# Kernel optimization log

Hardware: AMD Instinct MI355X
Metric: run time of the kernel (lower is better)

Reference implementation:

```python
import jax, jax.numpy as jnp
import numpy as np

B, IN_CH, OUT_CH = 4, 64, 128
N_HIGH, N_LOW = 163842, 40962
GROUPS, EPS, SLOPE = 4, 1e-5, 0.2


def setup_inputs() -> dict:
    key = jax.random.key(0)
    ks = jax.random.split(key, 6)
    x = jax.random.normal(ks[0], (B, IN_CH, N_HIGH), jnp.float32)
    pool_neigh = jax.random.randint(ks[1], (N_LOW * 7,), 0, N_HIGH, dtype=jnp.int32)
    conv_neigh = jax.random.randint(ks[2], (N_LOW * 7,), 0, N_LOW, dtype=jnp.int32)
    W1 = jax.random.normal(ks[3], (OUT_CH, 7 * IN_CH), jnp.float32) / np.float32(np.sqrt(7 * IN_CH))
    b1 = jnp.zeros((OUT_CH,), jnp.float32)
    W2 = jax.random.normal(ks[4], (OUT_CH, 7 * OUT_CH), jnp.float32) / np.float32(np.sqrt(7 * OUT_CH))
    b2 = jnp.zeros((OUT_CH,), jnp.float32)
    return dict(x=x, pool_neigh=pool_neigh, conv_neigh=conv_neigh,
                W1=W1, b1=b1, gn1_w=jnp.ones((OUT_CH,), jnp.float32), gn1_b=jnp.zeros((OUT_CH,), jnp.float32),
                W2=W2, b2=b2, gn2_w=jnp.ones((OUT_CH,), jnp.float32), gn2_b=jnp.zeros((OUT_CH,), jnp.float32))


def _mean_pool(x, pool_neigh):
    # x: (B, C, N_high); pool_neigh: (N_low*7,) -> (B, C, N_low)
    g = x[:, :, pool_neigh].reshape(x.shape[0], x.shape[1], -1, 7)
    return g.mean(axis=-1)


def _onering_conv(x, neigh, W, b):
    # x: (B, C, N); neigh: (N*7,); W: (O, 7*C). Torch Linear over gathered
    # (N*7, C).view(N, 7*C): neighbor-major, channel-minor concatenation.
    Bb, C, N = x.shape
    feat = x[:, :, neigh].reshape(Bb, C, N, 7)            # (B, C, N, 7)
    feat = jnp.transpose(feat, (0, 2, 3, 1)).reshape(Bb, N, 7 * C)  # (B, N, 7C)
    out = jnp.einsum('bnf,of->bno', feat, W) + b          # (B, N, O)
    return jnp.transpose(out, (0, 2, 1))                  # (B, O, N)


def _group_norm(x, w, b):
    # x: (B, C, N), normalize per (group, sample) over (C//G, N)
    Bb, C, N = x.shape
    xg = x.reshape(Bb, GROUPS, C // GROUPS, N)
    mu = xg.mean(axis=(2, 3), keepdims=True)
    var = ((xg - mu) ** 2).mean(axis=(2, 3), keepdims=True)
    xn = ((xg - mu) * jax.lax.rsqrt(var + EPS)).reshape(Bb, C, N)
    return xn * w[None, :, None] + b[None, :, None]


def _leaky_relu(x):
    return jnp.where(x >= 0, x, SLOPE * x)


def reference(x, pool_neigh, conv_neigh, W1, b1, gn1_w, gn1_b, W2, b2, gn2_w, gn2_b):
    h = _mean_pool(x, pool_neigh)
    h = _leaky_relu(_group_norm(_onering_conv(h, conv_neigh, W1, b1), gn1_w, gn1_b))
    h = _leaky_relu(_group_norm(_onering_conv(h, conv_neigh, W2, b2), gn2_w, gn2_b))
    return h
```

## Files before the change

### kernel.cpp

```cpp
#include <hip/hip_runtime.h>

#define B_SZ 4
#define IN_CH 64
#define OUT_CH 128
#define NHI 163842
#define NLO 40962
#define EPS_GN 1e-5f
#define SLOPE 0.2f

typedef __attribute__((ext_vector_type(8))) short short8;
typedef __attribute__((ext_vector_type(16))) float f32x16;

__device__ inline ushort f2bf(float f) {
    union { float f; unsigned u; } v; v.f = f;
    unsigned r = v.u + 0x7FFF + ((v.u >> 16) & 1);
    return (ushort)(r >> 16);
}
__device__ inline float bf2f(ushort h) {
    union { unsigned u; float f; } v; v.u = ((unsigned)h) << 16;
    return v.f;
}

__global__ void k_transpose_x(const float* __restrict__ x, ushort* __restrict__ xT) {
    __shared__ float t[64][65];
    const int b   = blockIdx.y;
    const int n0  = blockIdx.x * 64;
    const int tid = threadIdx.x;
    const int nq  = tid & 15;
    const int c0  = tid >> 4;
    const bool full = (n0 + 64) <= NHI;
    if (full) {
#pragma unroll
        for (int r = 0; r < 4; ++r) {
            int c = c0 + r * 16;
            float4 v = *(const float4*)&x[((long)b * IN_CH + c) * NHI + n0 + nq * 4];
            t[c][nq * 4 + 0] = v.x; t[c][nq * 4 + 1] = v.y;
            t[c][nq * 4 + 2] = v.z; t[c][nq * 4 + 3] = v.w;
        }
    } else {
        for (int r = 0; r < 4; ++r) {
            int c = c0 + r * 16;
            for (int e = 0; e < 4; ++e) {
                int n = n0 + nq * 4 + e;
                t[c][nq * 4 + e] = (n < NHI) ? x[((long)b * IN_CH + c) * NHI + n] : 0.f;
            }
        }
    }
    __syncthreads();
    const int n  = tid >> 2;
    const int cc = (tid & 3) * 16;
    if (n0 + n < NHI) {
        short8 o0, o1;
#pragma unroll
        for (int e = 0; e < 8; ++e) {
            o0[e] = (short)f2bf(t[cc + e][n]);
            o1[e] = (short)f2bf(t[cc + 8 + e][n]);
        }
        ushort* p = &xT[((long)b * NHI + n0 + n) * 64 + cc];
        *(short8*)p = o0;
        *(short8*)(p + 8) = o1;
    }
}

__global__ void k_prep_w(const float* __restrict__ W, ushort* __restrict__ Wb, int K) {
    int i = blockIdx.x * 256 + threadIdx.x;
    if (i >= K * 128) return;
    int k = i / 128, o = i % 128;
    int step = k >> 6, kk = k & 63, kg = kk >> 3, e = kk & 7;
    Wb[(((long)(step * 8 + kg) * 128 + o) * 8) + e] = f2bf(W[(long)o * K + k]);
}

__global__ void k_pool(const ushort* __restrict__ xT, const int* __restrict__ pn,
                       ushort* __restrict__ h1) {
    long t = (long)blockIdx.x * 256 + threadIdx.x;
    const long total = (long)B_SZ * NLO * 8;
    if (t >= total) return;
    int  cq = (int)(t & 7);
    long bn = t >> 3;
    int  n  = (int)(bn % NLO);
    int  b  = (int)(bn / NLO);
    float acc[8] = {};
#pragma unroll
    for (int j = 0; j < 7; ++j) {
        int idx = pn[n * 7 + j];
        short8 v = *(const short8*)&xT[((long)b * NHI + idx) * 64 + cq * 8];
#pragma unroll
        for (int e = 0; e < 8; ++e) acc[e] += bf2f((ushort)v[e]);
    }
    short8 o;
#pragma unroll
    for (int e = 0; e < 8; ++e) o[e] = (short)f2bf(acc[e] * (1.f / 7.f));
    *(short8*)&h1[bn * 64 + cq * 8] = o;
}

template <int CIN>
__global__ __launch_bounds__(256)
void k_conv_mfma(const ushort* __restrict__ src, const int* __restrict__ nbr,
                 const ushort* __restrict__ Wb, const float* __restrict__ bias,
                 ushort* __restrict__ out, float* __restrict__ part) {
    constexpr int K = 7 * CIN;
    constexpr int NSTEP = K / 64;
    __shared__ ushort Asm[8 * 64 * 8];
    __shared__ ushort Bsm[8 * 128 * 8];
    __shared__ float  red[4][4];

    const int b    = blockIdx.y;
    const int n0   = blockIdx.x * 64;
    const int tid  = threadIdx.x;
    const int lane = tid & 63;
    const int wave = tid >> 6;
    const int wr   = wave >> 1, wc = wave & 1;

    const int s_nn = tid >> 2;
    const int s_kq = tid & 3;
    int nrow = n0 + s_nn; if (nrow >= NLO) nrow = NLO - 1;
    const int* nbr_row = &nbr[nrow * 7];

    f32x16 acc0 = {}; f32x16 acc1 = {};
    const long srcb = (long)b * NLO * CIN;

    const int arow  = wr * 32 + (lane & 31);
    const int bcol0 = wc * 64 + (lane & 31);
    const int khalf = lane >> 5;

    for (int step = 0; step < NSTEP; ++step) {
        int j, cbase;
        if (CIN == 64) { j = step; cbase = 0; }
        else           { j = step >> 1; cbase = (step & 1) * 64; }
        int row = nbr_row[j];
        const ushort* sp = &src[srcb + (long)row * CIN + cbase + s_kq * 8];
        short8 a0 = *(const short8*)sp;
        short8 a1 = *(const short8*)(sp + 32);
        const ushort* wp = &Wb[(long)step * 8192 + tid * 32];
        short8 w0 = *(const short8*)(wp);
        short8 w1 = *(const short8*)(wp + 8);
        short8 w2 = *(const short8*)(wp + 16);
        short8 w3 = *(const short8*)(wp + 24);
        __syncthreads();
        *(short8*)&Asm[(s_kq * 64 + s_nn) * 8]       = a0;
        *(short8*)&Asm[((s_kq + 4) * 64 + s_nn) * 8] = a1;
        *(short8*)&Bsm[tid * 32]      = w0;
        *(short8*)&Bsm[tid * 32 + 8]  = w1;
        *(short8*)&Bsm[tid * 32 + 16] = w2;
        *(short8*)&Bsm[tid * 32 + 24] = w3;
        __syncthreads();
#pragma unroll
        for (int kh = 0; kh < 4; ++kh) {
            int kg = 2 * kh + khalf;
            short8 af  = *(const short8*)&Asm[(kg * 64 + arow) * 8];
            short8 bf0 = *(const short8*)&Bsm[(kg * 128 + bcol0) * 8];
            short8 bf1 = *(const short8*)&Bsm[(kg * 128 + bcol0 + 32) * 8];
            acc0 = __builtin_amdgcn_mfma_f32_32x32x16_bf16(af, bf0, acc0, 0, 0, 0);
            acc1 = __builtin_amdgcn_mfma_f32_32x32x16_bf16(af, bf1, acc1, 0, 0, 0);
        }
    }

    const float bias0 = bias[wc * 64 + (lane & 31)];
    const float bias1 = bias[wc * 64 + 32 + (lane & 31)];
    float s0 = 0.f, q0 = 0.f, s1 = 0.f, q1 = 0.f;
#pragma unroll
    for (int r = 0; r < 16; ++r) {
        int rrow = (r & 3) + 8 * (r >> 2) + 4 * khalf + wr * 32;
        int n = n0 + rrow;
        float v0 = acc0[r] + bias0;
        float v1 = acc1[r] + bias1;
        if (n < NLO) {
            long o = ((long)b * NLO + n) * 128 + wc * 64 + (lane & 31);
            out[o]      = f2bf(v0);
            out[o + 32] = f2bf(v1);
            s0 += v0; q0 += v0 * v0;
            s1 += v1; q1 += v1 * v1;
        }
    }
#pragma unroll
    for (int off = 32; off > 0; off >>= 1) {
        s0 += __shfl_down(s0, off); q0 += __shfl_down(q0, off);
        s1 += __shfl_down(s1, off); q1 += __shfl_down(q1, off);
    }
    if (lane == 0) { red[wave][0] = s0; red[wave][1] = q0; red[wave][2] = s1; red[wave][3] = q1; }
    __syncthreads();
    if (tid < 8) {
        int g = tid >> 1, isq = tid & 1;
        int wcg = g >> 1, ct = g & 1;
        float v = red[0 * 2 + wcg][ct * 2 + isq] + red[1 * 2 + wcg][ct * 2 + isq];
        part[(((long)b * gridDim.x + blockIdx.x) * 4 + g) * 2 + isq] = v;
    }
}

__global__ void k_finalize(const float* __restrict__ part, int nblk,
                           const float* __restrict__ w, const float* __restrict__ bb,
                           float* __restrict__ scale, float* __restrict__ shift) {
    const int b = blockIdx.x >> 2, g = blockIdx.x & 3;
    const int tid = threadIdx.x;
    float s = 0.f, ss = 0.f;
    for (int k = tid; k < nblk; k += 256) {
        s  += part[(((long)b * nblk + k) * 4 + g) * 2 + 0];
        ss += part[(((long)b * nblk + k) * 4 + g) * 2 + 1];
    }
#pragma unroll
    for (int off = 32; off > 0; off >>= 1) {
        s += __shfl_down(s, off); ss += __shfl_down(ss, off);
    }
    __shared__ float red[8];
    __shared__ float fin[2];
    const int wave = tid >> 6, lane = tid & 63;
    if (lane == 0) { red[wave * 2] = s; red[wave * 2 + 1] = ss; }
    __syncthreads();
    if (tid == 0) {
        float as = red[0] + red[2] + red[4] + red[6];
        float aq = red[1] + red[3] + red[5] + red[7];
        const float cnt = 32.f * NLO;
        float mu  = as / cnt;
        float var = aq / cnt - mu * mu;
        fin[0] = mu; fin[1] = rsqrtf(var + EPS_GN);
    }
    __syncthreads();
    if (tid < 32) {
        int c = g * 32 + tid;
        float sc = fin[1] * w[c];
        scale[b * 128 + c] = sc;
        shift[b * 128 + c] = bb[c] - fin[0] * sc;
    }
}

__global__ void k_gnapply(const ushort* __restrict__ y, const float* __restrict__ sc,
                          const float* __restrict__ sh, ushort* __restrict__ yp) {
    long t = (long)blockIdx.x * 256 + threadIdx.x;
    const long total = (long)B_SZ * NLO * 16;
    if (t >= total) return;
    int  c8 = (int)(t & 15);
    long bn = t >> 4;
    int  b  = (int)(bn / NLO);
    short8 v = *(const short8*)&y[bn * 128 + c8 * 8];
    short8 o;
#pragma unroll
    for (int e = 0; e < 8; ++e) {
        int c = c8 * 8 + e;
        float f = bf2f((ushort)v[e]) * sc[b * 128 + c] + sh[b * 128 + c];
        f = (f >= 0.f) ? f : SLOPE * f;
        o[e] = (short)f2bf(f);
    }
    *(short8*)&yp[bn * 128 + c8 * 8] = o;
}

__global__ void k_output(const ushort* __restrict__ y2, const float* __restrict__ scale,
                         const float* __restrict__ shift, float* __restrict__ out) {
    __shared__ float t[32][129];
    const int b   = blockIdx.y;
    const int n0  = blockIdx.x * 32;
    const int tid = threadIdx.x;
    const float* scb = &scale[b * 128];
    const float* shb = &shift[b * 128];
    const int c8 = (tid & 15) * 8;
#pragma unroll
    for (int r = 0; r < 2; ++r) {
        int nn = (tid >> 4) + r * 16;
        int n  = n0 + nn;
        if (n < NLO) {
            short8 v = *(const short8*)&y2[((long)b * NLO + n) * 128 + c8];
#pragma unroll
            for (int e = 0; e < 8; ++e) {
                int c = c8 + e;
                float f = bf2f((ushort)v[e]) * scb[c] + shb[c];
                t[nn][c] = (f >= 0.f) ? f : SLOPE * f;
            }
        } else {
#pragma unroll
            for (int e = 0; e < 8; ++e) t[nn][c8 + e] = 0.f;
        }
    }
    __syncthreads();
    const int n4 = (tid & 7) * 4;
    const bool full = (n0 + 32) <= NLO;
#pragma unroll
    for (int r = 0; r < 4; ++r) {
        int c = (tid >> 3) + r * 32;
        long o = ((long)b * 128 + c) * NLO + n0 + n4;
        if (full) {
            float2 v0 = make_float2(t[n4][c], t[n4 + 1][c]);
            float2 v1 = make_float2(t[n4 + 2][c], t[n4 + 3][c]);
            *(float2*)&out[o]     = v0;
            *(float2*)&out[o + 2] = v1;
        } else {
            for (int e = 0; e < 4; ++e)
                if (n0 + n4 + e < NLO) out[o + e] = t[n4 + e][c];
        }
    }
}

extern "C" void kernel_launch(void* const* d_in, const int* in_sizes, int n_in,
                              void* d_out, int out_size, void* d_ws, size_t ws_size,
                              hipStream_t stream) {
    const float* x   = (const float*)d_in[0];
    const int*   pn  = (const int*)d_in[1];
    const int*   cn  = (const int*)d_in[2];
    const float* W1  = (const float*)d_in[3];
    const float* b1  = (const float*)d_in[4];
    const float* g1w = (const float*)d_in[5];
    const float* g1b = (const float*)d_in[6];
    const float* W2  = (const float*)d_in[7];
    const float* b2  = (const float*)d_in[8];
    const float* g2w = (const float*)d_in[9];
    const float* g2b = (const float*)d_in[10];
    float* out = (float*)d_out;
    char*  base = (char*)d_ws;

    ushort* xT  = (ushort*)(base + 0);
    ushort* y1  = (ushort*)(base + 0);
    ushort* y1p = (ushort*)(base + 44000000);
    ushort* h1  = (ushort*)(base + 88000000);
    ushort* y2  = (ushort*)(base + 110000000);
    ushort* wb1 = (ushort*)(base + 152000000);
    ushort* wb2 = (ushort*)(base + 152200000);
    float*  p1  = (float*)(base + 152500000);
    float*  p2  = (float*)(base + 152600000);
    float*  sc1 = (float*)(base + 152700000);
    float*  sh1 = sc1 + 512;
    float*  sc2 = (float*)(base + 152710000);
    float*  sh2 = sc2 + 512;

    const int NBLK = (NLO + 63) / 64;

    k_transpose_x<<<dim3((NHI + 63) / 64, B_SZ), 256, 0, stream>>>(x, xT);
    k_prep_w<<<(448 * 128 + 255) / 256, 256, 0, stream>>>(W1, wb1, 448);
    k_prep_w<<<(896 * 128 + 255) / 256, 256, 0, stream>>>(W2, wb2, 896);
    k_pool<<<(int)(((long)B_SZ * NLO * 8 + 255) / 256), 256, 0, stream>>>(xT, pn, h1);
    k_conv_mfma<64><<<dim3(NBLK, B_SZ), 256, 0, stream>>>(h1, cn, wb1, b1, y1, p1);
    k_finalize<<<16, 256, 0, stream>>>(p1, NBLK, g1w, g1b, sc1, sh1);
    k_gnapply<<<(int)(((long)B_SZ * NLO * 16 + 255) / 256), 256, 0, stream>>>(y1, sc1, sh1, y1p);
    k_conv_mfma<128><<<dim3(NBLK, B_SZ), 256, 0, stream>>>(y1p, cn, wb2, b2, y2, p2);
    k_finalize<<<16, 256, 0, stream>>>(p2, NBLK, g2w, g2b, sc2, sh2);
    k_output<<<dim3((NLO + 31) / 32, B_SZ), 256, 0, stream>>>(y2, sc2, sh2, out);
}
```

Before: 267.5 us.

## Double-buffer conv MFMA tiles with register prefetch and widen to 128-row blocks

The one-ring conv kernel now handles 128 output rows per block with 512 threads instead of 64 rows with 256. Shared memory for the A and B tiles is double-buffered. Global loads for the next K step are issued into registers right after the barrier, so they overlap the current step's MFMAs, and each step needs one barrier instead of two. Each block loads its weight chunk once for twice as many rows, halving weight reloads, though the larger LDS footprint and thread count may reduce how many blocks fit on a CU. Leaky ReLU is also rewritten as fmaxf(f, slope*f) in the GroupNorm apply and output kernels.

```diff
diff --git a/kernel.cpp b/kernel.cpp
--- a/kernel.cpp
+++ b/kernel.cpp
@@ -94,18 +94,18 @@
 }
 
 template <int CIN>
-__global__ __launch_bounds__(256)
+__global__ __launch_bounds__(512, 4)
 void k_conv_mfma(const ushort* __restrict__ src, const int* __restrict__ nbr,
                  const ushort* __restrict__ Wb, const float* __restrict__ bias,
                  ushort* __restrict__ out, float* __restrict__ part) {
     constexpr int K = 7 * CIN;
     constexpr int NSTEP = K / 64;
-    __shared__ ushort Asm[8 * 64 * 8];
-    __shared__ ushort Bsm[8 * 128 * 8];
-    __shared__ float  red[4][4];
+    __shared__ ushort Asm[2][8 * 128 * 8];
+    __shared__ ushort Bsm[2][8 * 128 * 8];
+    __shared__ float  red[8][4];
 
     const int b    = blockIdx.y;
-    const int n0   = blockIdx.x * 64;
+    const int n0   = blockIdx.x * 128;
     const int tid  = threadIdx.x;
     const int lane = tid & 63;
     const int wave = tid >> 6;
@@ -116,40 +116,48 @@
     int nrow = n0 + s_nn; if (nrow >= NLO) nrow = NLO - 1;
     const int* nbr_row = &nbr[nrow * 7];
 
-    f32x16 acc0 = {}; f32x16 acc1 = {};
+    f32x16 acc0 = {}, acc1 = {};
     const long srcb = (long)b * NLO * CIN;
 
     const int arow  = wr * 32 + (lane & 31);
     const int bcol0 = wc * 64 + (lane & 31);
     const int khalf = lane >> 5;
 
+    short8 a0, a1, w0, w1;
+    {
+        int j = 0, cbase = 0;
+        const ushort* sp = &src[srcb + (long)nbr_row[j] * CIN + cbase + s_kq * 8];
+        a0 = *(const short8*)sp;
+        a1 = *(const short8*)(sp + 32);
+        const ushort* wp = &Wb[tid * 16];
+        w0 = *(const short8*)wp;
+        w1 = *(const short8*)(wp + 8);
+    }
+
     for (int step = 0; step < NSTEP; ++step) {
-        int j, cbase;
-        if (CIN == 64) { j = step; cbase = 0; }
-        else           { j = step >> 1; cbase = (step & 1) * 64; }
-        int row = nbr_row[j];
-        const ushort* sp = &src[srcb + (long)row * CIN + cbase + s_kq * 8];
-        short8 a0 = *(const short8*)sp;
-        short8 a1 = *(const short8*)(sp + 32);
-        const ushort* wp = &Wb[(long)step * 8192 + tid * 32];
-        short8 w0 = *(const short8*)(wp);
-        short8 w1 = *(const short8*)(wp + 8);
-        short8 w2 = *(const short8*)(wp + 16);
-        short8 w3 = *(const short8*)(wp + 24);
+        const int cur = step & 1;
+        *(short8*)&Asm[cur][(s_kq * 128 + s_nn) * 8]       = a0;
+        *(short8*)&Asm[cur][((s_kq + 4) * 128 + s_nn) * 8] = a1;
+        *(short8*)&Bsm[cur][tid * 16]     = w0;
+        *(short8*)&Bsm[cur][tid * 16 + 8] = w1;
         __syncthreads();
-        *(short8*)&Asm[(s_kq * 64 + s_nn) * 8]       = a0;
-        *(short8*)&Asm[((s_kq + 4) * 64 + s_nn) * 8] = a1;
-        *(short8*)&Bsm[tid * 32]      = w0;
-        *(short8*)&Bsm[tid * 32 + 8]  = w1;
-        *(short8*)&Bsm[tid * 32 + 16] = w2;
-        *(short8*)&Bsm[tid * 32 + 24] = w3;
-        __syncthreads();
+        if (step + 1 < NSTEP) {
+            int s = step + 1, j, cbase;
+            if (CIN == 64) { j = s; cbase = 0; }
+            else           { j = s >> 1; cbase = (s & 1) * 64; }
+            const ushort* sp = &src[srcb + (long)nbr_row[j] * CIN + cbase + s_kq * 8];
+            a0 = *(const short8*)sp;
+            a1 = *(const short8*)(sp + 32);
+            const ushort* wp = &Wb[(long)s * 8192 + tid * 16];
+            w0 = *(const short8*)wp;
+            w1 = *(const short8*)(wp + 8);
+        }
 #pragma unroll
         for (int kh = 0; kh < 4; ++kh) {
             int kg = 2 * kh + khalf;
-            short8 af  = *(const short8*)&Asm[(kg * 64 + arow) * 8];
-            short8 bf0 = *(const short8*)&Bsm[(kg * 128 + bcol0) * 8];
-            short8 bf1 = *(const short8*)&Bsm[(kg * 128 + bcol0 + 32) * 8];
+            short8 af  = *(const short8*)&Asm[cur][(kg * 128 + arow) * 8];
+            short8 bf0 = *(const short8*)&Bsm[cur][(kg * 128 + bcol0) * 8];
+            short8 bf1 = *(const short8*)&Bsm[cur][(kg * 128 + bcol0 + 32) * 8];
             acc0 = __builtin_amdgcn_mfma_f32_32x32x16_bf16(af, bf0, acc0, 0, 0, 0);
             acc1 = __builtin_amdgcn_mfma_f32_32x32x16_bf16(af, bf1, acc1, 0, 0, 0);
         }
@@ -182,7 +190,9 @@
     if (tid < 8) {
         int g = tid >> 1, isq = tid & 1;
         int wcg = g >> 1, ct = g & 1;
-        float v = red[0 * 2 + wcg][ct * 2 + isq] + red[1 * 2 + wcg][ct * 2 + isq];
+        float v = 0.f;
+#pragma unroll
+        for (int w = 0; w < 4; ++w) v += red[w * 2 + wcg][ct * 2 + isq];
         part[(((long)b * gridDim.x + blockIdx.x) * 4 + g) * 2 + isq] = v;
     }
 }
@@ -237,7 +247,7 @@
     for (int e = 0; e < 8; ++e) {
         int c = c8 * 8 + e;
         float f = bf2f((ushort)v[e]) * sc[b * 128 + c] + sh[b * 128 + c];
-        f = (f >= 0.f) ? f : SLOPE * f;
+        f = fmaxf(f, SLOPE * f);
         o[e] = (short)f2bf(f);
     }
     *(short8*)&yp[bn * 128 + c8 * 8] = o;
@@ -262,7 +272,7 @@
             for (int e = 0; e < 8; ++e) {
                 int c = c8 + e;
                 float f = bf2f((ushort)v[e]) * scb[c] + shb[c];
-                t[nn][c] = (f >= 0.f) ? f : SLOPE * f;
+                t[nn][c] = fmaxf(f, SLOPE * f);
             }
         } else {
 #pragma unroll
@@ -319,16 +329,16 @@
     float*  sc2 = (float*)(base + 152710000);
     float*  sh2 = sc2 + 512;
 
-    const int NBLK = (NLO + 63) / 64;
+    const int NBLK = (NLO + 127) / 128;
 
     k_transpose_x<<<dim3((NHI + 63) / 64, B_SZ), 256, 0, stream>>>(x, xT);
     k_prep_w<<<(448 * 128 + 255) / 256, 256, 0, stream>>>(W1, wb1, 448);
     k_prep_w<<<(896 * 128 + 255) / 256, 256, 0, stream>>>(W2, wb2, 896);
     k_pool<<<(int)(((long)B_SZ * NLO * 8 + 255) / 256), 256, 0, stream>>>(xT, pn, h1);
-    k_conv_mfma<64><<<dim3(NBLK, B_SZ), 256, 0, stream>>>(h1, cn, wb1, b1, y1, p1);
+    k_conv_mfma<64><<<dim3(NBLK, B_SZ), 512, 0, stream>>>(h1, cn, wb1, b1, y1, p1);
     k_finalize<<<16, 256, 0, stream>>>(p1, NBLK, g1w, g1b, sc1, sh1);
     k_gnapply<<<(int)(((long)B_SZ * NLO * 16 + 255) / 256), 256, 0, stream>>>(y1, sc1, sh1, y1p);
-    k_conv_mfma<128><<<dim3(NBLK, B_SZ), 256, 0, stream>>>(y1p, cn, wb2, b2, y2, p2);
+    k_conv_mfma<128><<<dim3(NBLK, B_SZ), 512, 0, stream>>>(y1p, cn, wb2, b2, y2, p2);
     k_finalize<<<16, 256, 0, stream>>>(p2, NBLK, g2w, g2b, sc2, sh2);
     k_output<<<dim3((NLO + 31) / 32, B_SZ), 256, 0, stream>>>(y2, sc2, sh2, out);
 }
```

After: 248.0 us. 1.08x faster.
